# Kernel optimization log

Measured on AMD Instinct MI355X. Metric: run time of the kernel, lower is better.

The kernel has to match this reference:

```python
import jax, jax.numpy as jnp
import numpy as np
from jax import lax

B, C_IN, H, W = 8, 64, 256, 256
HEADS, QD, U, VD = 4, 16, 1, 32  # heads, query_depth, intra_depth, v_depth = out_ch//heads
EPS = 1e-5  # BatchNorm eps (eval mode: running_mean=0, running_var=1)


def setup_inputs() -> dict:
    key = jax.random.key(0)
    ks = jax.random.split(key, 10)
    x = jax.random.normal(ks[0], (B, C_IN, H, W), dtype=jnp.float32)
    Wq = jax.random.normal(ks[1], (QD * HEADS, C_IN), dtype=jnp.float32) * 0.05
    gq = jax.random.normal(ks[2], (QD * HEADS,), dtype=jnp.float32) * 0.1 + 1.0
    bq = jax.random.normal(ks[3], (QD * HEADS,), dtype=jnp.float32) * 0.05
    Wk = jax.random.normal(ks[4], (QD * U, C_IN), dtype=jnp.float32) * 0.05
    Wv = jax.random.normal(ks[5], (VD * U, C_IN), dtype=jnp.float32) * 0.05
    gv = jax.random.normal(ks[6], (VD * U,), dtype=jnp.float32) * 0.1 + 1.0
    bv = jax.random.normal(ks[7], (VD * U,), dtype=jnp.float32) * 0.05
    Wp = jax.random.normal(ks[8], (QD, U, 1, 3, 3), dtype=jnp.float32) * 0.1  # Conv3d (1,3,3)
    bp = jax.random.normal(ks[9], (QD,), dtype=jnp.float32) * 0.05
    return {"x": x, "Wq": Wq, "gq": gq, "bq": bq, "Wk": Wk, "Wv": Wv,
            "gv": gv, "bv": bv, "Wp": Wp, "bp": bp}


def _bn_eval(y, gamma, beta):
    # BatchNorm in eval mode with running_mean=0, running_var=1
    s = gamma / jnp.sqrt(1.0 + EPS)
    return y * s[None, :, None, None] + beta[None, :, None, None]


def reference(x, Wq, gq, bq, Wk, Wv, gv, bv, Wp, bp):
    b, c, h, w = x.shape
    n = h * w
    # 1x1 convs as channel matmuls
    q = jnp.einsum('oc,bchw->bohw', Wq, x)
    q = _bn_eval(q, gq, bq).reshape(b, HEADS, QD, n)           # b h k n
    k = jnp.einsum('oc,bchw->bohw', Wk, x).reshape(b, U, QD, n)  # b u k m
    v = jnp.einsum('oc,bchw->bohw', Wv, x)
    v = _bn_eval(v, gv, bv).reshape(b, U, VD, n)               # b u v m
    k = jax.nn.softmax(k, axis=-1)
    # content lambda: global context
    lam_c = jnp.einsum('bukm,buvm->bkv', k, v)                 # b k v
    Yc = jnp.einsum('bhkn,bkv->bhvn', q, lam_c)
    # position lambda: 3D conv over (v-depth, h, w) with kernel (1,3,3)
    v_p = v.reshape(b, U, VD, h, w)                            # N C D H W (D = v-depth)
    lam_p = lax.conv_general_dilated(
        v_p, Wp, window_strides=(1, 1, 1),
        padding=[(0, 0), (1, 1), (1, 1)],
        dimension_numbers=('NCDHW', 'OIDHW', 'NCDHW'))
    lam_p = lam_p + bp[None, :, None, None, None]              # b k v h w
    Yp = jnp.einsum('bhkn,bkvn->bhvn', q, lam_p.reshape(b, QD, VD, n))
    Y = Yc + Yp                                                # b h v n
    return Y.reshape(b, HEADS * VD, h, w)
```

## Files before the change

kernel.cpp:

```cpp
#include <hip/hip_runtime.h>
#include <hip/hip_bf16.h>
#include <cstddef>

#define BB    8
#define CIN   64
#define HH    256
#define WW    256
#define NN    65536
#define NP    (BB*NN)
#define QC    64
#define KC    16
#define VC    32
#define HEADS 4
#define QD    16

#define WALL_OFF 0
#define BQ_OFF 7168
#define BV_OFF 7232
#define WP_OFF 7264
#define BP_OFF 7408
#define S_OFF  7424
#define M_OFF  7552
#define SMALL_END 11648
#define FLAG_OFF 12000
#define BF_BASE 65536

typedef __hip_bfloat16 bf16;
typedef __attribute__((ext_vector_type(8))) short short8;
typedef __attribute__((ext_vector_type(4))) short short4v;
typedef __attribute__((ext_vector_type(4))) float f32x4;

#define MFMA16(a, b, c) __builtin_amdgcn_mfma_f32_16x16x32_bf16((a), (b), (c), 0, 0, 0)

__device__ __forceinline__ short f2bf_s(float f) {
    bf16 h = (bf16)f;
    return __builtin_bit_cast(short, h);
}
__device__ __forceinline__ float bf2f(short u) {
    unsigned x = ((unsigned)(unsigned short)u) << 16;
    return __builtin_bit_cast(float, x);
}

__global__ void k_detect(const unsigned short* __restrict xu, int* __restrict flag) {
    if (threadIdx.x == 0 && blockIdx.x == 0) {
        int big = 0, zero = 0;
        for (int i = 0; i < 256; ++i) {
            unsigned short u = xu[i];
            int e = (u >> 7) & 0xFF;
            big  += (e >= 134);
            zero += (u == 0);
        }
        *flag = (big > 4 || zero > 64) ? 1 : 0;
    }
}

__device__ __forceinline__ float ldin(const void* p, int i, int isf) {
    return isf ? ((const float*)p)[i] : (float)(((const bf16*)p)[i]);
}

__global__ void k_prep(const void* __restrict wq, const void* __restrict gq,
                       const void* __restrict bq, const void* __restrict wk,
                       const void* __restrict wv, const void* __restrict gv,
                       const void* __restrict bv, const void* __restrict wp,
                       const void* __restrict bp, float* __restrict wf,
                       const int* __restrict flag) {
    int t = threadIdx.x;
    int isf = *flag;
    float rs = rsqrtf(1.0f + 1e-5f);
    for (int i = t; i < 4096; i += 256)
        wf[WALL_OFF + i] = ldin(wq, i, isf) * (ldin(gq, i>>6, isf) * rs);
    for (int i = t; i < 1024; i += 256)
        wf[WALL_OFF + 4096 + i] = ldin(wk, i, isf);
    for (int i = t; i < 2048; i += 256)
        wf[WALL_OFF + 5120 + i] = ldin(wv, i, isf) * (ldin(gv, i>>6, isf) * rs);
    for (int i = t; i < 64;   i += 256) wf[BQ_OFF+i] = ldin(bq, i, isf);
    for (int i = t; i < 32;   i += 256) wf[BV_OFF+i] = ldin(bv, i, isf);
    for (int i = t; i < 144;  i += 256) wf[WP_OFF+i] = ldin(wp, i, isf);
    for (int i = t; i < 16;   i += 256) wf[BP_OFF+i] = ldin(bp, i, isf);
    for (int i = t; i < SMALL_END - S_OFF; i += 256) wf[S_OFF + i] = 0.0f;
}

#define TPW 4
__global__ __launch_bounds__(256) void k_qkv(const void* __restrict x,
        const float* __restrict wf, const int* __restrict flag,
        bf16* __restrict qws2, bf16* __restrict ekws, bf16* __restrict vws) {
    const int lane = threadIdx.x & 63;
    const int m = lane & 15, g = lane >> 4;
    const int wave = blockIdx.x * 4 + (threadIdx.x >> 6);
    const int px0 = wave * (TPW * 16);
    const int b = px0 >> 16;
    const int n0 = px0 & 0xFFFF;
    const int isf = *flag;

    short8 a[7][2];
    #pragma unroll
    for (int mt = 0; mt < 7; ++mt)
        #pragma unroll
        for (int kh = 0; kh < 2; ++kh) {
            const float* wr = wf + WALL_OFF + (mt * 16 + m) * 64 + kh * 32 + g * 8;
            short8 t;
            #pragma unroll
            for (int i = 0; i < 8; ++i) t[i] = f2bf_s(wr[i]);
            a[mt][kh] = t;
        }

    f32x4 bias[7];
    #pragma unroll
    for (int mt = 0; mt < 4; ++mt)
        #pragma unroll
        for (int r = 0; r < 4; ++r) bias[mt][r] = wf[BQ_OFF + mt * 16 + g * 4 + r];
    #pragma unroll
    for (int r = 0; r < 4; ++r) bias[4][r] = 0.0f;
    #pragma unroll
    for (int mt = 5; mt < 7; ++mt)
        #pragma unroll
        for (int r = 0; r < 4; ++r) bias[mt][r] = wf[BV_OFF + (mt - 5) * 16 + g * 4 + r];

    #pragma unroll
    for (int it = 0; it < TPW; ++it) {
        const int n = n0 + it * 16 + m;
        const size_t p = (size_t)px0 + it * 16 + m;

        short8 bf0, bf1;
        if (isf) {
            const float* xp = (const float*)x + (size_t)b * CIN * NN
                            + (size_t)g * 8 * NN + n;
            #pragma unroll
            for (int i = 0; i < 8; ++i) bf0[i] = f2bf_s(xp[(size_t)i * NN]);
            #pragma unroll
            for (int i = 0; i < 8; ++i) bf1[i] = f2bf_s(xp[(size_t)(32 + i) * NN]);
        } else {
            const unsigned short* xp = (const unsigned short*)x + (size_t)b * CIN * NN
                                     + (size_t)g * 8 * NN + n;
            #pragma unroll
            for (int i = 0; i < 8; ++i) bf0[i] = (short)xp[(size_t)i * NN];
            #pragma unroll
            for (int i = 0; i < 8; ++i) bf1[i] = (short)xp[(size_t)(32 + i) * NN];
        }

        f32x4 acc[7];
        #pragma unroll
        for (int mt = 0; mt < 7; ++mt) {
            acc[mt] = MFMA16(a[mt][0], bf0, bias[mt]);
            acc[mt] = MFMA16(a[mt][1], bf1, acc[mt]);
        }

        bf16* qp = qws2 + p * 64;
        #pragma unroll
        for (int mt = 0; mt < 4; ++mt) {
            short4v pk;
            #pragma unroll
            for (int r = 0; r < 4; ++r) pk[r] = f2bf_s(acc[mt][r]);
            *(short4v*)(qp + mt * 16 + g * 4) = pk;
        }
        #pragma unroll
        for (int r = 0; r < 4; ++r)
            ekws[(size_t)(g * 4 + r) * NP + p] = (bf16)__expf(acc[4][r]);
        #pragma unroll
        for (int mt = 0; mt < 2; ++mt)
            #pragma unroll
            for (int r = 0; r < 4; ++r)
                vws[(size_t)(mt * 16 + g * 4 + r) * NP + p] = (bf16)acc[5 + mt][r];
    }
}

__global__ __launch_bounds__(256) void k_lamc(const bf16* __restrict ekws,
        const bf16* __restrict vws, float* __restrict Sg, float* __restrict Mg) {
    __shared__ float MM[4][512];
    __shared__ float SS[4][16];
    const int b = blockIdx.y, chunk = blockIdx.x;
    const int t = threadIdx.x, w = t >> 6, lane = t & 63;
    const int m = lane & 15, g = lane >> 4;
    const size_t px0 = (size_t)b * NN + (size_t)chunk * 1024 + (size_t)w * 256;

    f32x4 acc0 = {0.f, 0.f, 0.f, 0.f}, acc1 = {0.f, 0.f, 0.f, 0.f};
    float s = 0.0f;
    #pragma unroll
    for (int st = 0; st < 8; ++st) {
        const size_t p = px0 + st * 32 + g * 8;
        short8 afr = *(const short8*)(ekws + (size_t)m * NP + p);
        short8 b0  = *(const short8*)(vws + (size_t)m * NP + p);
        short8 b1  = *(const short8*)(vws + (size_t)(16 + m) * NP + p);
        acc0 = MFMA16(afr, b0, acc0);
        acc1 = MFMA16(afr, b1, acc1);
        #pragma unroll
        for (int i = 0; i < 8; ++i) s += bf2f(afr[i]);
    }
    s += __shfl_xor(s, 16);
    s += __shfl_xor(s, 32);
    if (g == 0) SS[w][m] = s;
    #pragma unroll
    for (int r = 0; r < 4; ++r) {
        MM[w][(g * 4 + r) * 32 + m]      = acc0[r];
        MM[w][(g * 4 + r) * 32 + 16 + m] = acc1[r];
    }
    __syncthreads();
    for (int i = t; i < 512; i += 256) {
        float v4 = MM[0][i] + MM[1][i] + MM[2][i] + MM[3][i];
        atomicAdd(&Mg[b * 512 + i], v4);
    }
    if (t < 16) atomicAdd(&Sg[b * 16 + t], SS[0][t] + SS[1][t] + SS[2][t] + SS[3][t]);
}

__global__ __launch_bounds__(256) void k_out(const bf16* __restrict qws2,
        const bf16* __restrict vws, const float* __restrict wf,
        const float* __restrict Sg, const float* __restrict Mg,
        const int* __restrict flag, void* __restrict outv) {
    const int y = blockIdx.x, b = blockIdx.y, xc = threadIdx.x;
    const int isf = *flag;
    __shared__ float As[512];
    __shared__ float WPs[144];
    __shared__ unsigned short VS[16 * 3 * 272];

    for (int i = threadIdx.x; i < 512; i += 256) {
        int k = i & 15, v = i >> 4;
        As[i] = Mg[b * 512 + k * 32 + v] / Sg[b * 16 + k] + wf[BP_OFF + k];
    }
    if (threadIdx.x < 144) WPs[threadIdx.x] = wf[WP_OFF + threadIdx.x];
    __syncthreads();

    const size_t pix = (size_t)b * NN + (size_t)y * WW + xc;
    const short8* qrow = (const short8*)(qws2 + pix * 64);
    float qf[64];
    #pragma unroll
    for (int j = 0; j < 8; ++j) {
        short8 qv = qrow[j];
        #pragma unroll
        for (int e = 0; e < 8; ++e) qf[j * 8 + e] = bf2f(qv[e]);
    }

    float g4[HEADS][9];
    #pragma unroll
    for (int h = 0; h < HEADS; ++h)
        #pragma unroll
        for (int tn = 0; tn < 9; ++tn) g4[h][tn] = 0.0f;
    #pragma unroll
    for (int k = 0; k < 16; ++k)
        #pragma unroll
        for (int tn = 0; tn < 9; ++tn) {
            float w = WPs[k * 9 + tn];
            #pragma unroll
            for (int h = 0; h < HEADS; ++h) g4[h][tn] += qf[h * 16 + k] * w;
        }

    for (int half = 0; half < 2; ++half) {
        #pragma unroll
        for (int kk = 0; kk < 6; ++kk) {
            int idx = threadIdx.x + kk * 256;
            int pair = idx >> 5, off = (idx & 31) * 8;
            int c = pair & 15, j = pair >> 4;
            int yy = y + j - 1;
            short8 val = {0, 0, 0, 0, 0, 0, 0, 0};
            if (yy >= 0 && yy < HH)
                val = *(const short8*)(vws + (size_t)(half * 16 + c) * NP
                                       + (size_t)b * NN + (size_t)yy * WW + off);
            *(short8*)&VS[c * 816 + j * 272 + 8 + off] = val;
        }
        if (threadIdx.x < 96) {
            int pr = threadIdx.x >> 1, side = threadIdx.x & 1;
            int c = pr & 15, j = pr >> 4;
            VS[c * 816 + j * 272 + (side ? 264 : 7)] = 0;
        }
        __syncthreads();

        #pragma unroll 2
        for (int vl = 0; vl < 16; ++vl) {
            const int vc = half * 16 + vl;
            float vnf[9];
            const unsigned short* vb = &VS[vl * 816 + 8 + xc - 1];
            #pragma unroll
            for (int j = 0; j < 3; ++j)
                #pragma unroll
                for (int dx = 0; dx < 3; ++dx)
                    vnf[j * 3 + dx] = bf2f((short)vb[j * 272 + dx]);
            float Ak[16];
            const f32x4* ap = (const f32x4*)&As[vc * 16];
            #pragma unroll
            for (int qq = 0; qq < 4; ++qq) {
                f32x4 a4 = ap[qq];
                #pragma unroll
                for (int e = 0; e < 4; ++e) Ak[qq * 4 + e] = a4[e];
            }
            #pragma unroll
            for (int h = 0; h < HEADS; ++h) {
                float acc = 0.0f;
                #pragma unroll
                for (int k = 0; k < 16; ++k) acc += qf[h * 16 + k] * Ak[k];
                #pragma unroll
                for (int tn = 0; tn < 9; ++tn) acc += g4[h][tn] * vnf[tn];
                size_t idx2 = ((size_t)(b * HEADS + h) * VC + vc) * NN
                            + (size_t)y * WW + xc;
                if (isf) ((float*)outv)[idx2] = acc;
                else     ((bf16*)outv)[idx2] = (bf16)acc;
            }
        }
        __syncthreads();
    }
}

extern "C" void kernel_launch(void* const* d_in, const int* in_sizes, int n_in,
                              void* d_out, int out_size, void* d_ws, size_t ws_size,
                              hipStream_t stream) {
    float* wf = (float*)d_ws;
    int* flag = (int*)wf + FLAG_OFF;
    bf16* qws2 = (bf16*)((char*)d_ws + BF_BASE);
    bf16* ekws = qws2 + (size_t)QC * NP;
    bf16* vws  = ekws + (size_t)KC * NP;

    k_detect<<<1, 64, 0, stream>>>((const unsigned short*)d_in[0], flag);
    k_prep<<<1, 256, 0, stream>>>(d_in[1], d_in[2], d_in[3], d_in[4], d_in[5],
                                  d_in[6], d_in[7], d_in[8], d_in[9], wf, flag);
    k_qkv<<<NP / 256, 256, 0, stream>>>(d_in[0], wf, flag, qws2, ekws, vws);
    k_lamc<<<dim3(64, BB), 256, 0, stream>>>(ekws, vws, wf + S_OFF, wf + M_OFF);
    k_out<<<dim3(HH, BB), 256, 0, stream>>>(qws2, vws, wf, wf + S_OFF, wf + M_OFF,
                                            flag, d_out);
}
```

Measured before the change: 599.9 us.

## Split output kernel by half-row and head group, shrink qkv and lamc work per block

k_out now gives each block half an image row, and splits its 256 threads into two head groups. Each thread keeps only 32 q values and 18 conv-weight accumulators, which cuts register pressure. All 32 v channels are staged in LDS once with a single barrier, replacing the two-pass half loop. k_qkv halves the tiles per wave and k_lamc uses chunks four times smaller, so both launch more blocks for better occupancy and parallelism. In exchange, k_lamc performs more atomics, k_out loads more halo, and the k_qkv weight fragments are reloaded more often.

```diff
diff --git a/kernel.cpp b/kernel.cpp
--- a/kernel.cpp
+++ b/kernel.cpp
@@ -80,7 +80,7 @@
     for (int i = t; i < SMALL_END - S_OFF; i += 256) wf[S_OFF + i] = 0.0f;
 }
 
-#define TPW 4
+#define TPW 2
 __global__ __launch_bounds__(256) void k_qkv(const void* __restrict x,
         const float* __restrict wf, const int* __restrict flag,
         bf16* __restrict qws2, bf16* __restrict ekws, bf16* __restrict vws) {
@@ -164,6 +164,7 @@
     }
 }
 
+#define LCHUNK 256
 __global__ __launch_bounds__(256) void k_lamc(const bf16* __restrict ekws,
         const bf16* __restrict vws, float* __restrict Sg, float* __restrict Mg) {
     __shared__ float MM[4][512];
@@ -171,12 +172,12 @@
     const int b = blockIdx.y, chunk = blockIdx.x;
     const int t = threadIdx.x, w = t >> 6, lane = t & 63;
     const int m = lane & 15, g = lane >> 4;
-    const size_t px0 = (size_t)b * NN + (size_t)chunk * 1024 + (size_t)w * 256;
+    const size_t px0 = (size_t)b * NN + (size_t)chunk * LCHUNK + (size_t)w * 64;
 
     f32x4 acc0 = {0.f, 0.f, 0.f, 0.f}, acc1 = {0.f, 0.f, 0.f, 0.f};
     float s = 0.0f;
     #pragma unroll
-    for (int st = 0; st < 8; ++st) {
+    for (int st = 0; st < 2; ++st) {
         const size_t p = px0 + st * 32 + g * 8;
         short8 afr = *(const short8*)(ekws + (size_t)m * NP + p);
         short8 b0  = *(const short8*)(vws + (size_t)m * NP + p);
@@ -206,95 +207,93 @@
         const bf16* __restrict vws, const float* __restrict wf,
         const float* __restrict Sg, const float* __restrict Mg,
         const int* __restrict flag, void* __restrict outv) {
-    const int y = blockIdx.x, b = blockIdx.y, xc = threadIdx.x;
+    const int y = blockIdx.x >> 1, xh = blockIdx.x & 1, b = blockIdx.y;
+    const int tid = threadIdx.x;
+    const int pxl = tid & 127, hg = tid >> 7;
+    const int px0 = xh * 128;
     const int isf = *flag;
+
     __shared__ float As[512];
     __shared__ float WPs[144];
-    __shared__ unsigned short VS[16 * 3 * 272];
-
-    for (int i = threadIdx.x; i < 512; i += 256) {
+    __shared__ unsigned short VS[32 * 3 * 144];
+
+    for (int i = tid; i < 512; i += 256) {
         int k = i & 15, v = i >> 4;
         As[i] = Mg[b * 512 + k * 32 + v] / Sg[b * 16 + k] + wf[BP_OFF + k];
     }
-    if (threadIdx.x < 144) WPs[threadIdx.x] = wf[WP_OFF + threadIdx.x];
+    if (tid < 144) WPs[tid] = wf[WP_OFF + tid];
+
+    #pragma unroll
+    for (int kk = 0; kk < 7; ++kk) {
+        int idx = tid + kk * 256;
+        if (idx < 1728) {
+            int c = idx / 54, rem = idx - c * 54;
+            int j = rem / 18, i = rem - j * 18;
+            int yy = y + j - 1;
+            int x0 = px0 - 8 + i * 8;
+            short8 val = {0, 0, 0, 0, 0, 0, 0, 0};
+            if (yy >= 0 && yy < HH && x0 >= 0 && x0 <= WW - 8)
+                val = *(const short8*)(vws + (size_t)c * NP + (size_t)b * NN
+                                       + (size_t)yy * WW + x0);
+            *(short8*)&VS[(c * 3 + j) * 144 + i * 8] = val;
+        }
+    }
     __syncthreads();
 
-    const size_t pix = (size_t)b * NN + (size_t)y * WW + xc;
-    const short8* qrow = (const short8*)(qws2 + pix * 64);
-    float qf[64];
-    #pragma unroll
-    for (int j = 0; j < 8; ++j) {
+    const size_t pix = (size_t)b * NN + (size_t)y * WW + px0 + pxl;
+    const short8* qrow = (const short8*)(qws2 + pix * 64) + hg * 4;
+    float qf[32];
+    #pragma unroll
+    for (int j = 0; j < 4; ++j) {
         short8 qv = qrow[j];
         #pragma unroll
         for (int e = 0; e < 8; ++e) qf[j * 8 + e] = bf2f(qv[e]);
     }
 
-    float g4[HEADS][9];
-    #pragma unroll
-    for (int h = 0; h < HEADS; ++h)
-        #pragma unroll
-        for (int tn = 0; tn < 9; ++tn) g4[h][tn] = 0.0f;
+    float g4[2][9];
+    #pragma unroll
+    for (int hl = 0; hl < 2; ++hl)
+        #pragma unroll
+        for (int tn = 0; tn < 9; ++tn) g4[hl][tn] = 0.0f;
     #pragma unroll
     for (int k = 0; k < 16; ++k)
         #pragma unroll
         for (int tn = 0; tn < 9; ++tn) {
             float w = WPs[k * 9 + tn];
-            #pragma unroll
-            for (int h = 0; h < HEADS; ++h) g4[h][tn] += qf[h * 16 + k] * w;
-        }
-
-    for (int half = 0; half < 2; ++half) {
-        #pragma unroll
-        for (int kk = 0; kk < 6; ++kk) {
-            int idx = threadIdx.x + kk * 256;
-            int pair = idx >> 5, off = (idx & 31) * 8;
-            int c = pair & 15, j = pair >> 4;
-            int yy = y + j - 1;
-            short8 val = {0, 0, 0, 0, 0, 0, 0, 0};
-            if (yy >= 0 && yy < HH)
-                val = *(const short8*)(vws + (size_t)(half * 16 + c) * NP
-                                       + (size_t)b * NN + (size_t)yy * WW + off);
-            *(short8*)&VS[c * 816 + j * 272 + 8 + off] = val;
-        }
-        if (threadIdx.x < 96) {
-            int pr = threadIdx.x >> 1, side = threadIdx.x & 1;
-            int c = pr & 15, j = pr >> 4;
-            VS[c * 816 + j * 272 + (side ? 264 : 7)] = 0;
-        }
-        __syncthreads();
-
-        #pragma unroll 2
-        for (int vl = 0; vl < 16; ++vl) {
-            const int vc = half * 16 + vl;
-            float vnf[9];
-            const unsigned short* vb = &VS[vl * 816 + 8 + xc - 1];
-            #pragma unroll
-            for (int j = 0; j < 3; ++j)
-                #pragma unroll
-                for (int dx = 0; dx < 3; ++dx)
-                    vnf[j * 3 + dx] = bf2f((short)vb[j * 272 + dx]);
-            float Ak[16];
-            const f32x4* ap = (const f32x4*)&As[vc * 16];
-            #pragma unroll
-            for (int qq = 0; qq < 4; ++qq) {
-                f32x4 a4 = ap[qq];
-                #pragma unroll
-                for (int e = 0; e < 4; ++e) Ak[qq * 4 + e] = a4[e];
-            }
-            #pragma unroll
-            for (int h = 0; h < HEADS; ++h) {
-                float acc = 0.0f;
-                #pragma unroll
-                for (int k = 0; k < 16; ++k) acc += qf[h * 16 + k] * Ak[k];
-                #pragma unroll
-                for (int tn = 0; tn < 9; ++tn) acc += g4[h][tn] * vnf[tn];
-                size_t idx2 = ((size_t)(b * HEADS + h) * VC + vc) * NN
-                            + (size_t)y * WW + xc;
-                if (isf) ((float*)outv)[idx2] = acc;
-                else     ((bf16*)outv)[idx2] = (bf16)acc;
-            }
-        }
-        __syncthreads();
+            g4[0][tn] += qf[k] * w;
+            g4[1][tn] += qf[16 + k] * w;
+        }
+
+    const size_t obase = ((size_t)(b * HEADS + hg * 2) * VC) * NN
+                       + (size_t)y * WW + px0 + pxl;
+    #pragma unroll 2
+    for (int vc = 0; vc < VC; ++vc) {
+        float vnf[9];
+        const unsigned short* vb = &VS[vc * 3 * 144 + 7 + pxl];
+        #pragma unroll
+        for (int j = 0; j < 3; ++j)
+            #pragma unroll
+            for (int dx = 0; dx < 3; ++dx)
+                vnf[j * 3 + dx] = bf2f((short)vb[j * 144 + dx]);
+        float Ak[16];
+        const f32x4* ap = (const f32x4*)&As[vc * 16];
+        #pragma unroll
+        for (int qq = 0; qq < 4; ++qq) {
+            f32x4 a4 = ap[qq];
+            #pragma unroll
+            for (int e = 0; e < 4; ++e) Ak[qq * 4 + e] = a4[e];
+        }
+        #pragma unroll
+        for (int hl = 0; hl < 2; ++hl) {
+            float acc = 0.0f;
+            #pragma unroll
+            for (int k = 0; k < 16; ++k) acc += qf[hl * 16 + k] * Ak[k];
+            #pragma unroll
+            for (int tn = 0; tn < 9; ++tn) acc += g4[hl][tn] * vnf[tn];
+            size_t idx2 = obase + ((size_t)hl * VC + vc) * NN;
+            if (isf) ((float*)outv)[idx2] = acc;
+            else     ((bf16*)outv)[idx2] = (bf16)acc;
+        }
     }
 }
 
@@ -310,8 +309,8 @@
     k_detect<<<1, 64, 0, stream>>>((const unsigned short*)d_in[0], flag);
     k_prep<<<1, 256, 0, stream>>>(d_in[1], d_in[2], d_in[3], d_in[4], d_in[5],
                                   d_in[6], d_in[7], d_in[8], d_in[9], wf, flag);
-    k_qkv<<<NP / 256, 256, 0, stream>>>(d_in[0], wf, flag, qws2, ekws, vws);
-    k_lamc<<<dim3(64, BB), 256, 0, stream>>>(ekws, vws, wf + S_OFF, wf + M_OFF);
-    k_out<<<dim3(HH, BB), 256, 0, stream>>>(qws2, vws, wf, wf + S_OFF, wf + M_OFF,
-                                            flag, d_out);
-}
+    k_qkv<<<NP / 128, 256, 0, stream>>>(d_in[0], wf, flag, qws2, ekws, vws);
+    k_lamc<<<dim3(NN / LCHUNK, BB), 256, 0, stream>>>(ekws, vws, wf + S_OFF, wf + M_OFF);
+    k_out<<<dim3(2 * HH, BB), 256, 0, stream>>>(qws2, vws, wf, wf + S_OFF, wf + M_OFF,
+                                                flag, d_out);
+}
```

Result: faster. 529.7 us (-11.7%).
